# Kernel tuning notes

Hardware: AMD Instinct MI355X
Metric: run time of the kernel (lower is better)

## Reference

```python
import jax, jax.numpy as jnp
import numpy as np

D = 4096       # hidden_dim
L = 4          # num_iter
NEG = -1e9     # masked-softmax fill


def setup_inputs() -> dict:
    key = jax.random.key(0)
    ks = jax.random.split(key, 7)
    s_d = 1.0 / np.sqrt(D)
    s_2d = 1.0 / np.sqrt(2 * D)
    pi = np.float32(np.pi)
    concept_embed = jax.random.normal(ks[0], (54, D), jnp.float32)
    gat_W  = jax.random.normal(ks[1], (L, D, D), jnp.float32) * s_d     # HieGAT linear (no bias)
    att_if = jax.random.normal(ks[2], (L, 2 * D), jnp.float32) * s_2d   # Linear(2D,1) weight as vector
    att_fd = jax.random.normal(ks[3], (L, 2 * D), jnp.float32) * s_2d
    att_dr = jax.random.normal(ks[4], (L, 2 * D), jnp.float32) * s_2d
    meta_W = jax.random.normal(ks[5], (L, D, D), jnp.float32) * s_d     # MetapathAggr linear
    edge_embed = jax.random.uniform(ks[6], (3, D // 2), jnp.float32, minval=-pi, maxval=pi)
    # tree_structure[2] = [3,2,3,2,2] (facets per domain), tree_structure[3] = [3]*12 (ideos per facet)
    parent_of_facet = jnp.asarray(np.repeat(np.arange(5), [3, 2, 3, 2, 2]), jnp.int32)   # [12]
    parent_of_ideo = jnp.asarray(np.repeat(np.arange(12), 3), jnp.int32)                 # [36]
    return dict(concept_embed=concept_embed, gat_W=gat_W, att_if=att_if, att_fd=att_fd,
                att_dr=att_dr, meta_W=meta_W, edge_embed=edge_embed,
                parent_of_facet=parent_of_facet, parent_of_ideo=parent_of_ideo)


def _leaky(x):
    return jnp.where(x > 0, x, 0.01 * x)


def _attn_level(center, children, parent_idx, w):
    # center [P,D], children [C,D], parent_idx [C] -> aggregated centers [P,D]
    P = center.shape[0]
    s_self = _leaky(jnp.concatenate([center, center], axis=1) @ w)                 # [P]
    s_child = _leaky(jnp.concatenate([center[parent_idx], children], axis=1) @ w)  # [C]
    mask = parent_idx[None, :] == jnp.arange(P)[:, None]                           # [P,C]
    scores = jnp.concatenate([s_self[:, None], jnp.where(mask, s_child[None, :], NEG)], axis=1)
    a = jax.nn.softmax(scores, axis=1)                                             # [P,C+1]
    return a[:, :1] * center + a[:, 1:] @ children


def reference(concept_embed, gat_W, att_if, att_fd, att_dr, meta_W, edge_embed,
              parent_of_facet, parent_of_ideo):
    e_r, e_i = jnp.cos(edge_embed), jnp.sin(edge_embed)   # [3, D/2]
    pf = parent_of_facet
    pi_ = parent_of_ideo
    x = concept_embed
    for i in range(gat_W.shape[0]):
        # --- HieGAT layer: bottom-up attention aggregation ---
        h = x @ gat_W[i].T                                 # [54,D]
        root, dom, fac, ideo = h[0:1], h[1:6], h[6:18], h[18:54]
        fac_new = _attn_level(fac, ideo, pi_, att_if[i])
        dom_new = _attn_level(dom, fac_new, pf, att_fd[i])
        root_new = _attn_level(root, dom_new, jnp.zeros(5, jnp.int32), att_dr[i])
        x = jnp.concatenate([root_new, dom_new, fac_new, ideo], axis=0)
        # --- Metapath aggregation: top-down complex rotations ---
        h = x @ meta_W[i].T                                # [54,D]
        hr, hi = jnp.split(h, 2, axis=1)                   # each [54, D/2]
        rr, ri = hr[0:1], hi[0:1]
        dr = hr[1:6] + (rr * e_r[0] - ri * e_i[0])
        di = hi[1:6] + (rr * e_i[0] + ri * e_r[0])
        fr = hr[6:18] + (dr[pf] * e_r[1] - di[pf] * e_i[1])
        fi = hi[6:18] + (dr[pf] * e_i[1] + di[pf] * e_r[1])
        ir = hr[18:54] + (fr[pi_] * e_r[2] - fi[pi_] * e_i[2])
        ii = hi[18:54] + (fr[pi_] * e_i[2] + fi[pi_] * e_r[2])
        x = jnp.concatenate([
            h[0:1],
            jnp.concatenate([dr, di], axis=1) / 2,
            jnp.concatenate([fr, fi], axis=1) / 3,
            jnp.concatenate([ir, ii], axis=1) / 4,
        ], axis=0)
    return x
```

## Files before the change

### kernel.cpp

```cpp
#include <hip/hip_runtime.h>
#include <hip/hip_bf16.h>

#define DIM 4096
#define HROWS 54
#define HSZ (54 * 4096)
#define SPLITK 16
#define KSLICE 256

typedef __attribute__((ext_vector_type(4))) float  f32x4;
typedef __attribute__((ext_vector_type(8))) short  s16x8;
typedef __attribute__((ext_vector_type(4))) short  s16x4;

__device__ __forceinline__ short f2bf(float f) {
    union { __hip_bfloat16 h; short s; } u;
    u.h = __float2bfloat16(f);
    return u.s;
}
__device__ __forceinline__ float bf2f(short s) {
    union { __hip_bfloat16 h; short s; } u;
    u.s = s;
    return __bfloat162float(u.h);
}
__device__ __forceinline__ float leaky(float x) { return x > 0.f ? x : 0.01f * x; }

__device__ __forceinline__ void split8(const f32x4& c0, const f32x4& c1,
                                       s16x8& h, s16x8& l) {
#pragma unroll
    for (int j = 0; j < 4; ++j) {
        short h0 = f2bf(c0[j]); h[j]     = h0; l[j]     = f2bf(c0[j] - bf2f(h0));
        short h1 = f2bf(c1[j]); h[4 + j] = h1; l[4 + j] = f2bf(c1[j] - bf2f(h1));
    }
}

__global__ __launch_bounds__(256) void prep_g(const float* __restrict__ ce,
                                              const float* __restrict__ edge,
                                              short* __restrict__ xh, short* __restrict__ xl,
                                              short* __restrict__ hbh, short* __restrict__ hbl,
                                              float* __restrict__ er, float* __restrict__ ei)
{
    const int idx = blockIdx.x * 256 + threadIdx.x;
    const int row = idx >> 12;
    if (row < HROWS) {
        const float v = ce[idx];
        const short h = f2bf(v);
        xh[idx] = h; xl[idx] = f2bf(v - bf2f(h));
    } else {
        xh[idx] = 0; xl[idx] = 0; hbh[idx] = 0; hbl[idx] = 0;
    }
    if (idx < 3 * 2048) {
        const float e = edge[idx];
        er[idx] = cosf(e);
        ei[idx] = sinf(e);
    }
}

__global__ __launch_bounds__(256) void gemm_g(const short* __restrict__ Ah,
                                              const short* __restrict__ Al,
                                              const float* __restrict__ W,
                                              float* __restrict__ outp)
{
    __shared__ short lhi[64 * 256];
    __shared__ short llo[64 * 256];

    const int tid  = threadIdx.x;
    const int lane = tid & 63;
    const int wv   = tid >> 6;
    const int nb   = blockIdx.x & 31;
    const int ks   = blockIdx.x >> 5;
    const int l15  = lane & 15;
    const int lk8  = lane >> 4;
    const int koff = ks * KSLICE;

    for (int u = tid; u < 64 * 32; u += 256) {
        const int row  = u >> 5;
        const int c    = u & 31;
        const int slot = c ^ (row & 7);
        *(s16x8*)&lhi[row * 256 + slot * 8] =
            *(const s16x8*)(Ah + (size_t)row * DIM + koff + c * 8);
        *(s16x8*)&llo[row * 256 + slot * 8] =
            *(const s16x8*)(Al + (size_t)row * DIM + koff + c * 8);
    }
    __syncthreads();

    const int ncolA = nb * 128 + wv * 16 + l15;
    const int ncolB = ncolA + 64;
    const float* wpA = W + (size_t)ncolA * DIM + koff + lk8 * 8;
    const float* wpB = W + (size_t)ncolB * DIM + koff + lk8 * 8;

    f32x4 accA0 = {0.f,0.f,0.f,0.f}, accA1 = {0.f,0.f,0.f,0.f};
    f32x4 accA2 = {0.f,0.f,0.f,0.f}, accA3 = {0.f,0.f,0.f,0.f};
    f32x4 accB0 = {0.f,0.f,0.f,0.f}, accB1 = {0.f,0.f,0.f,0.f};
    f32x4 accB2 = {0.f,0.f,0.f,0.f}, accB3 = {0.f,0.f,0.f,0.f};

#define WLD(P, KB)                                                           \
    const f32x4 P##a0 = *(const f32x4*)(wpA + (KB)*64);                      \
    const f32x4 P##a1 = *(const f32x4*)(wpA + (KB)*64 + 4);                  \
    const f32x4 P##a2 = *(const f32x4*)(wpA + (KB)*64 + 32);                 \
    const f32x4 P##a3 = *(const f32x4*)(wpA + (KB)*64 + 36);                 \
    const f32x4 P##b0 = *(const f32x4*)(wpB + (KB)*64);                      \
    const f32x4 P##b1 = *(const f32x4*)(wpB + (KB)*64 + 4);                  \
    const f32x4 P##b2 = *(const f32x4*)(wpB + (KB)*64 + 32);                 \
    const f32x4 P##b3 = *(const f32x4*)(wpB + (KB)*64 + 36);

#define CKK(WA0, WA1, WB0, WB1, KB, KK)                                      \
    {   const int sl_ = (((KB)*8 + (KK)*4 + lk8) ^ (l15 & 7)) * 8;           \
        const s16x8 a0h = *(const s16x8*)&lhi[( 0 + l15)*256 + sl_];         \
        const s16x8 a1h = *(const s16x8*)&lhi[(16 + l15)*256 + sl_];         \
        const s16x8 a2h = *(const s16x8*)&lhi[(32 + l15)*256 + sl_];         \
        const s16x8 a3h = *(const s16x8*)&lhi[(48 + l15)*256 + sl_];         \
        const s16x8 a0l = *(const s16x8*)&llo[( 0 + l15)*256 + sl_];         \
        const s16x8 a1l = *(const s16x8*)&llo[(16 + l15)*256 + sl_];         \
        const s16x8 a2l = *(const s16x8*)&llo[(32 + l15)*256 + sl_];         \
        const s16x8 a3l = *(const s16x8*)&llo[(48 + l15)*256 + sl_];         \
        s16x8 bhA, blA, bhB, blB;                                            \
        split8(WA0, WA1, bhA, blA);                                          \
        split8(WB0, WB1, bhB, blB);                                          \
        accA0 = __builtin_amdgcn_mfma_f32_16x16x32_bf16(a0h, bhA, accA0, 0, 0, 0); \
        accA1 = __builtin_amdgcn_mfma_f32_16x16x32_bf16(a1h, bhA, accA1, 0, 0, 0); \
        accA2 = __builtin_amdgcn_mfma_f32_16x16x32_bf16(a2h, bhA, accA2, 0, 0, 0); \
        accA3 = __builtin_amdgcn_mfma_f32_16x16x32_bf16(a3h, bhA, accA3, 0, 0, 0); \
        accA0 = __builtin_amdgcn_mfma_f32_16x16x32_bf16(a0l, bhA, accA0, 0, 0, 0); \
        accA1 = __builtin_amdgcn_mfma_f32_16x16x32_bf16(a1l, bhA, accA1, 0, 0, 0); \
        accA2 = __builtin_amdgcn_mfma_f32_16x16x32_bf16(a2l, bhA, accA2, 0, 0, 0); \
        accA3 = __builtin_amdgcn_mfma_f32_16x16x32_bf16(a3l, bhA, accA3, 0, 0, 0); \
        accA0 = __builtin_amdgcn_mfma_f32_16x16x32_bf16(a0h, blA, accA0, 0, 0, 0); \
        accA1 = __builtin_amdgcn_mfma_f32_16x16x32_bf16(a1h, blA, accA1, 0, 0, 0); \
        accA2 = __builtin_amdgcn_mfma_f32_16x16x32_bf16(a2h, blA, accA2, 0, 0, 0); \
        accA3 = __builtin_amdgcn_mfma_f32_16x16x32_bf16(a3h, blA, accA3, 0, 0, 0); \
        accB0 = __builtin_amdgcn_mfma_f32_16x16x32_bf16(a0h, bhB, accB0, 0, 0, 0); \
        accB1 = __builtin_amdgcn_mfma_f32_16x16x32_bf16(a1h, bhB, accB1, 0, 0, 0); \
        accB2 = __builtin_amdgcn_mfma_f32_16x16x32_bf16(a2h, bhB, accB2, 0, 0, 0); \
        accB3 = __builtin_amdgcn_mfma_f32_16x16x32_bf16(a3h, bhB, accB3, 0, 0, 0); \
        accB0 = __builtin_amdgcn_mfma_f32_16x16x32_bf16(a0l, bhB, accB0, 0, 0, 0); \
        accB1 = __builtin_amdgcn_mfma_f32_16x16x32_bf16(a1l, bhB, accB1, 0, 0, 0); \
        accB2 = __builtin_amdgcn_mfma_f32_16x16x32_bf16(a2l, bhB, accB2, 0, 0, 0); \
        accB3 = __builtin_amdgcn_mfma_f32_16x16x32_bf16(a3l, bhB, accB3, 0, 0, 0); \
        accB0 = __builtin_amdgcn_mfma_f32_16x16x32_bf16(a0h, blB, accB0, 0, 0, 0); \
        accB1 = __builtin_amdgcn_mfma_f32_16x16x32_bf16(a1h, blB, accB1, 0, 0, 0); \
        accB2 = __builtin_amdgcn_mfma_f32_16x16x32_bf16(a2h, blB, accB2, 0, 0, 0); \
        accB3 = __builtin_amdgcn_mfma_f32_16x16x32_bf16(a3h, blB, accB3, 0, 0, 0); }

    WLD(w0_, 0) WLD(w1_, 1)
    CKK(w0_a0, w0_a1, w0_b0, w0_b1, 0, 0)
    CKK(w0_a2, w0_a3, w0_b2, w0_b3, 0, 1)
    WLD(w2_, 2)
    CKK(w1_a0, w1_a1, w1_b0, w1_b1, 1, 0)
    CKK(w1_a2, w1_a3, w1_b2, w1_b3, 1, 1)
    WLD(w3_, 3)
    CKK(w2_a0, w2_a1, w2_b0, w2_b1, 2, 0)
    CKK(w2_a2, w2_a3, w2_b2, w2_b3, 2, 1)
    CKK(w3_a0, w3_a1, w3_b0, w3_b1, 3, 0)
    CKK(w3_a2, w3_a3, w3_b2, w3_b3, 3, 1)

#undef WLD
#undef CKK

    float* op = outp + (size_t)ks * HSZ;
#pragma unroll
    for (int mt = 0; mt < 4; ++mt) {
        const f32x4 a = (mt == 0) ? accA0 : (mt == 1) ? accA1 : (mt == 2) ? accA2 : accA3;
        const f32x4 b = (mt == 0) ? accB0 : (mt == 1) ? accB1 : (mt == 2) ? accB2 : accB3;
#pragma unroll
        for (int r = 0; r < 4; ++r) {
            const int m = mt * 16 + lk8 * 4 + r;
            if (m < HROWS) {
                op[(size_t)m * DIM + ncolA] = a[r];
                op[(size_t)m * DIM + ncolB] = b[r];
            }
        }
    }
}

__global__ __launch_bounds__(256) void p2_g(const float* __restrict__ hpart,
                                            const float* __restrict__ wA,
                                            const float* __restrict__ wB,
                                            const float* __restrict__ wC,
                                            short* __restrict__ hbh, short* __restrict__ hbl,
                                            float* __restrict__ dotp)
{
    const int vb  = blockIdx.x;
    const int tid = threadIdx.x;
    const int i   = vb * 1024 + tid * 4;
    const int col = i & (DIM - 1);
    f32x4 s = {0.f,0.f,0.f,0.f};
#pragma unroll
    for (int sl = 0; sl < SPLITK; ++sl) s += *(const f32x4*)(hpart + (size_t)sl * HSZ + i);

    s16x4 vh, vl;
#pragma unroll
    for (int j = 0; j < 4; ++j) {
        const short h = f2bf(s[j]);
        vh[j] = h; vl[j] = f2bf(s[j] - bf2f(h));
    }
    *(s16x4*)(hbh + i) = vh;
    *(s16x4*)(hbl + i) = vl;

    float a0=0,a1=0,a2=0,a3=0,a4=0,a5=0;
#pragma unroll
    for (int j = 0; j < 4; ++j) {
        const float sv = s[j];
        const int c = col + j;
        a0 += sv * wA[c]; a1 += sv * wA[DIM + c];
        a2 += sv * wB[c]; a3 += sv * wB[DIM + c];
        a4 += sv * wC[c]; a5 += sv * wC[DIM + c];
    }
#pragma unroll
    for (int off = 32; off > 0; off >>= 1) {
        a0 += __shfl_down(a0, off); a1 += __shfl_down(a1, off);
        a2 += __shfl_down(a2, off); a3 += __shfl_down(a3, off);
        a4 += __shfl_down(a4, off); a5 += __shfl_down(a5, off);
    }
    if ((tid & 63) == 0) {
        float* d = dotp + ((size_t)vb * 4 + (tid >> 6)) * 6;
        d[0]=a0; d[1]=a1; d[2]=a2; d[3]=a3; d[4]=a4; d[5]=a5;
    }
}

__global__ __launch_bounds__(256) void p45_g(const float* __restrict__ hpart,
                                             const float* __restrict__ dotp,
                                             const float* __restrict__ er,
                                             const float* __restrict__ ei,
                                             short* __restrict__ xh, short* __restrict__ xl,
                                             float* __restrict__ xo, int last)
{
    const int b   = blockIdx.x;
    const int tid = threadIdx.x;
    __shared__ float gs[HROWS][16];
    __shared__ float ds[324];
    __shared__ float Ts[54][54];
    __shared__ float ad0[5], adc[12], ar[6], fdot3[12], fdot5[12], ddot5[5];

    for (int x = tid; x < HROWS * 16; x += 256) {
        const int row = x >> 4;
        const int c   = x & 15;
        const int gj  = (c < 8) ? (b * 8 + c) : (2048 + b * 8 + (c - 8));
        float s = 0.f;
#pragma unroll
        for (int sl = 0; sl < SPLITK; ++sl)
            s += hpart[(size_t)sl * HSZ + (size_t)row * DIM + gj];
        gs[row][c] = s;
    }

    for (int x = tid; x < 324; x += 256) {
        const int r_ = x / 6, v = x % 6;
        float s = 0.f;
#pragma unroll
        for (int u = 0; u < 16; ++u) s += dotp[(size_t)(r_ * 16 + u) * 6 + v];
        ds[x] = s;
    }
    for (int i = tid; i < 54 * 54; i += 256) ((float*)Ts)[i] = 0.f;
    __syncthreads();

    if (tid < 12) {
        const int p = tid;
        const float u = ds[(6+p)*6 + 0];
        const float ss = leaky(u + ds[(6+p)*6 + 1]);
        float sc[3], mx = ss;
#pragma unroll
        for (int j = 0; j < 3; ++j) { sc[j] = leaky(u + ds[(18+3*p+j)*6 + 1]); mx = fmaxf(mx, sc[j]); }
        float e0 = expf(ss - mx), s = e0, ec[3];
#pragma unroll
        for (int j = 0; j < 3; ++j) { ec[j] = expf(sc[j] - mx); s += ec[j]; }
        const float inv = 1.f / s;
        const float a0 = e0 * inv;
        float f3 = a0 * ds[(6+p)*6 + 3];
        float f5 = a0 * ds[(6+p)*6 + 5];
        Ts[6+p][6+p] = a0;
#pragma unroll
        for (int j = 0; j < 3; ++j) {
            const float a = ec[j] * inv;
            Ts[6+p][18+3*p+j] = a;
            f3 += a * ds[(18+3*p+j)*6 + 3];
            f5 += a * ds[(18+3*p+j)*6 + 5];
        }
        fdot3[p] = f3; fdot5[p] = f5;
    }
    __syncthreads();

    if (tid < 5) {
        const int p = tid;
        const int cstart[5] = {0,3,5,8,10};
        const int ccnt[5]   = {3,2,3,2,2};
        const float u = ds[(1+p)*6 + 2];
        const float ss = leaky(u + ds[(1+p)*6 + 3]);
        const int n = ccnt[p], c0 = cstart[p];
        float mx = ss, sc[3];
        for (int j = 0; j < n; ++j) { sc[j] = leaky(u + fdot3[c0+j]); mx = fmaxf(mx, sc[j]); }
        float e0 = expf(ss - mx), s = e0, ec[3];
        for (int j = 0; j < n; ++j) { ec[j] = expf(sc[j] - mx); s += ec[j]; }
        const float inv = 1.f / s;
        ad0[p] = e0 * inv;
        float d5 = ad0[p] * ds[(1+p)*6 + 5];
        for (int j = 0; j < n; ++j) {
            const float a = ec[j] * inv;
            adc[c0+j] = a;
            d5 += a * fdot5[c0+j];
        }
        ddot5[p] = d5;
    }
    __syncthreads();

    if (tid == 0) {
        const float u = ds[0*6 + 4];
        const float ss = leaky(u + ds[0*6 + 5]);
        float mx = ss, sc[5];
#pragma unroll
        for (int d = 0; d < 5; ++d) { sc[d] = leaky(u + ddot5[d]); mx = fmaxf(mx, sc[d]); }
        float e0 = expf(ss - mx), s = e0, ec[5];
#pragma unroll
        for (int d = 0; d < 5; ++d) { ec[d] = expf(sc[d] - mx); s += ec[d]; }
        const float inv = 1.f / s;
        ar[0] = e0 * inv;
#pragma unroll
        for (int d = 0; d < 5; ++d) ar[1+d] = ec[d] * inv;
    }
    for (int q = tid; q < 36; q += 256) Ts[18+q][18+q] = 1.f;
    __syncthreads();

    if (tid < 54) {
        const int j = tid;
        const int cstart[5] = {0,3,5,8,10};
        const int ccnt[5]   = {3,2,3,2,2};
        for (int p = 0; p < 5; ++p) {
            float t = ad0[p] * ((j == 1+p) ? 1.f : 0.f);
            for (int c = cstart[p]; c < cstart[p] + ccnt[p]; ++c) t += adc[c] * Ts[6+c][j];
            Ts[1+p][j] = t;
        }
    }
    __syncthreads();
    if (tid < 54) {
        float t = ar[0] * ((tid == 0) ? 1.f : 0.f);
        for (int d = 0; d < 5; ++d) t += ar[1+d] * Ts[1+d][tid];
        Ts[0][tid] = t;
    }
    __syncthreads();

    const int p  = tid & 7;
    const int rq = tid >> 3;
    const int j  = b * 8 + p;
    const int jj = j + 2048;
    constexpr int PF[12] = {0,0,0,1,1,2,2,2,3,3,4,4};

    const float er0 = er[j],        ei0 = ei[j];
    const float er1 = er[2048 + j], ei1 = ei[2048 + j];
    const float er2 = er[4096 + j], ei2 = ei[4096 + j];

    float a0r = 0.f, a0i = 0.f;
#pragma unroll 6
    for (int k = 0; k < HROWS; ++k) {
        const float t0 = Ts[0][k];
        a0r += t0 * gs[k][p];
        a0i += t0 * gs[k][p + 8];
    }
    const float rr = a0r, ri = a0i;

    for (int r = rq; r < HROWS; r += 32) {
        float vr, vi, scale;
        if (r == 0) {
            vr = rr; vi = ri; scale = 1.f;
        } else {
            int row1, row2 = 0;
            if (r < 6)       { row1 = r; }
            else if (r < 18) { const int c = r - 6;      row1 = 1 + PF[c]; row2 = r; }
            else             { const int c = (r - 18)/3; row1 = 1 + PF[c]; row2 = 6 + c; }

            float a1r = 0.f, a1i = 0.f;
#pragma unroll 6
            for (int k = 0; k < HROWS; ++k) {
                const float t1 = Ts[row1][k];
                a1r += t1 * gs[k][p];
                a1i += t1 * gs[k][p + 8];
            }
            const float dr = a1r + rr * er0 - ri * ei0;
            const float di = a1i + rr * ei0 + ri * er0;
            if (r < 6) {
                vr = dr; vi = di; scale = 0.5f;
            } else {
                float a2r = 0.f, a2i = 0.f;
#pragma unroll 6
                for (int k = 0; k < HROWS; ++k) {
                    const float t2 = Ts[row2][k];
                    a2r += t2 * gs[k][p];
                    a2i += t2 * gs[k][p + 8];
                }
                const float fr = a2r + dr * er1 - di * ei1;
                const float fi = a2i + dr * ei1 + di * er1;
                if (r < 18) {
                    vr = fr; vi = fi; scale = 1.f / 3.f;
                } else {
                    vr = gs[r][p]     + fr * er2 - fi * ei2;
                    vi = gs[r][p + 8] + fr * ei2 + fi * er2;
                    scale = 0.25f;
                }
            }
        }
        vr *= scale; vi *= scale;
        if (last) {
            xo[(size_t)r * DIM + j]  = vr;
            xo[(size_t)r * DIM + jj] = vi;
        } else {
            const short h0 = f2bf(vr);
            xh[(size_t)r * DIM + j] = h0;
            xl[(size_t)r * DIM + j] = f2bf(vr - bf2f(h0));
            const short h1 = f2bf(vi);
            xh[(size_t)r * DIM + jj] = h1;
            xl[(size_t)r * DIM + jj] = f2bf(vi - bf2f(h1));
        }
    }
}

extern "C" void kernel_launch(void* const* d_in, const int* in_sizes, int n_in,
                              void* d_out, int out_size, void* d_ws, size_t ws_size,
                              hipStream_t stream)
{
    const float* ce    = (const float*)d_in[0];
    const float* gatW  = (const float*)d_in[1];
    const float* attif = (const float*)d_in[2];
    const float* attfd = (const float*)d_in[3];
    const float* attdr = (const float*)d_in[4];
    const float* metaW = (const float*)d_in[5];
    const float* edge  = (const float*)d_in[6];
    float* out = (float*)d_out;

    char* w = (char*)d_ws;
    float* hpart = (float*)w;   w += (size_t)SPLITK * HSZ * 4;
    float* dotp  = (float*)w;   w += 6144 * 4;
    float* er    = (float*)w;   w += 3 * 2048 * 4;
    float* ei    = (float*)w;   w += 3 * 2048 * 4;
    short* xbfh  = (short*)w;   w += (size_t)64 * DIM * 2;
    short* xbfl  = (short*)w;   w += (size_t)64 * DIM * 2;
    short* hbfh  = (short*)w;   w += (size_t)64 * DIM * 2;
    short* hbfl  = (short*)w;   w += (size_t)64 * DIM * 2;

    hipLaunchKernelGGL(prep_g, dim3(1024), dim3(256), 0, stream,
                       ce, edge, xbfh, xbfl, hbfh, hbfl, er, ei);

    for (int i = 0; i < 4; ++i) {
        hipLaunchKernelGGL(gemm_g, dim3(512), dim3(256), 0, stream,
                           xbfh, xbfl, gatW + (size_t)i * DIM * DIM, hpart);
        hipLaunchKernelGGL(p2_g, dim3(216), dim3(256), 0, stream,
                           hpart, attif + (size_t)i * 2 * DIM, attfd + (size_t)i * 2 * DIM,
                           attdr + (size_t)i * 2 * DIM, hbfh, hbfl, dotp);
        hipLaunchKernelGGL(gemm_g, dim3(512), dim3(256), 0, stream,
                           hbfh, hbfl, metaW + (size_t)i * DIM * DIM, hpart);
        hipLaunchKernelGGL(p45_g, dim3(256), dim3(256), 0, stream,
                           hpart, dotp, er, ei, xbfh, xbfl, out, (i == 3) ? 1 : 0);
    }
}
```

Measured before the change: 259.0 us.

## Fuse activation bf16 split into GEMM staging, halve split-K, drop prep kernel

The GEMM now reads fp32 activations directly and does the hi/lo bf16 split while staging into shared memory. The prep kernel and the separate bf16 activation buffers are removed, and cos/sin of the edge embeddings are computed inside p45. Split-K drops from 16 to 8 and each block covers 64 columns over a 512-wide K slice in two staged halves, which halves the partial-sum traffic reduced in p2/p45. The cost is redundant split work across the 64 column blocks, fp32 activation reads that are twice as wide, extra syncs, and fewer accumulators per wave.

```diff
diff --git a/kernel.cpp b/kernel.cpp
--- a/kernel.cpp
+++ b/kernel.cpp
@@ -4,12 +4,11 @@
 #define DIM 4096
 #define HROWS 54
 #define HSZ (54 * 4096)
-#define SPLITK 16
-#define KSLICE 256
+#define SPLITK 8
+#define KSLICE 512
 
 typedef __attribute__((ext_vector_type(4))) float  f32x4;
 typedef __attribute__((ext_vector_type(8))) short  s16x8;
-typedef __attribute__((ext_vector_type(4))) short  s16x4;
 
 __device__ __forceinline__ short f2bf(float f) {
     union { __hip_bfloat16 h; short s; } u;
@@ -32,30 +31,7 @@
     }
 }
 
-__global__ __launch_bounds__(256) void prep_g(const float* __restrict__ ce,
-                                              const float* __restrict__ edge,
-                                              short* __restrict__ xh, short* __restrict__ xl,
-                                              short* __restrict__ hbh, short* __restrict__ hbl,
-                                              float* __restrict__ er, float* __restrict__ ei)
-{
-    const int idx = blockIdx.x * 256 + threadIdx.x;
-    const int row = idx >> 12;
-    if (row < HROWS) {
-        const float v = ce[idx];
-        const short h = f2bf(v);
-        xh[idx] = h; xl[idx] = f2bf(v - bf2f(h));
-    } else {
-        xh[idx] = 0; xl[idx] = 0; hbh[idx] = 0; hbl[idx] = 0;
-    }
-    if (idx < 3 * 2048) {
-        const float e = edge[idx];
-        er[idx] = cosf(e);
-        ei[idx] = sinf(e);
-    }
-}
-
-__global__ __launch_bounds__(256) void gemm_g(const short* __restrict__ Ah,
-                                              const short* __restrict__ Al,
+__global__ __launch_bounds__(256) void gemm_g(const float* __restrict__ Asrc,
                                               const float* __restrict__ W,
                                               float* __restrict__ outp)
 {
@@ -65,108 +41,94 @@
     const int tid  = threadIdx.x;
     const int lane = tid & 63;
     const int wv   = tid >> 6;
-    const int nb   = blockIdx.x & 31;
-    const int ks   = blockIdx.x >> 5;
+    const int nb   = blockIdx.x & 63;
+    const int ks   = blockIdx.x >> 6;
     const int l15  = lane & 15;
     const int lk8  = lane >> 4;
     const int koff = ks * KSLICE;
 
-    for (int u = tid; u < 64 * 32; u += 256) {
-        const int row  = u >> 5;
-        const int c    = u & 31;
-        const int slot = c ^ (row & 7);
-        *(s16x8*)&lhi[row * 256 + slot * 8] =
-            *(const s16x8*)(Ah + (size_t)row * DIM + koff + c * 8);
-        *(s16x8*)&llo[row * 256 + slot * 8] =
-            *(const s16x8*)(Al + (size_t)row * DIM + koff + c * 8);
-    }
-    __syncthreads();
-
-    const int ncolA = nb * 128 + wv * 16 + l15;
-    const int ncolB = ncolA + 64;
-    const float* wpA = W + (size_t)ncolA * DIM + koff + lk8 * 8;
-    const float* wpB = W + (size_t)ncolB * DIM + koff + lk8 * 8;
-
-    f32x4 accA0 = {0.f,0.f,0.f,0.f}, accA1 = {0.f,0.f,0.f,0.f};
-    f32x4 accA2 = {0.f,0.f,0.f,0.f}, accA3 = {0.f,0.f,0.f,0.f};
-    f32x4 accB0 = {0.f,0.f,0.f,0.f}, accB1 = {0.f,0.f,0.f,0.f};
-    f32x4 accB2 = {0.f,0.f,0.f,0.f}, accB3 = {0.f,0.f,0.f,0.f};
-
-#define WLD(P, KB)                                                           \
-    const f32x4 P##a0 = *(const f32x4*)(wpA + (KB)*64);                      \
-    const f32x4 P##a1 = *(const f32x4*)(wpA + (KB)*64 + 4);                  \
-    const f32x4 P##a2 = *(const f32x4*)(wpA + (KB)*64 + 32);                 \
-    const f32x4 P##a3 = *(const f32x4*)(wpA + (KB)*64 + 36);                 \
-    const f32x4 P##b0 = *(const f32x4*)(wpB + (KB)*64);                      \
-    const f32x4 P##b1 = *(const f32x4*)(wpB + (KB)*64 + 4);                  \
-    const f32x4 P##b2 = *(const f32x4*)(wpB + (KB)*64 + 32);                 \
-    const f32x4 P##b3 = *(const f32x4*)(wpB + (KB)*64 + 36);
-
-#define CKK(WA0, WA1, WB0, WB1, KB, KK)                                      \
-    {   const int sl_ = (((KB)*8 + (KK)*4 + lk8) ^ (l15 & 7)) * 8;           \
-        const s16x8 a0h = *(const s16x8*)&lhi[( 0 + l15)*256 + sl_];         \
-        const s16x8 a1h = *(const s16x8*)&lhi[(16 + l15)*256 + sl_];         \
-        const s16x8 a2h = *(const s16x8*)&lhi[(32 + l15)*256 + sl_];         \
-        const s16x8 a3h = *(const s16x8*)&lhi[(48 + l15)*256 + sl_];         \
-        const s16x8 a0l = *(const s16x8*)&llo[( 0 + l15)*256 + sl_];         \
-        const s16x8 a1l = *(const s16x8*)&llo[(16 + l15)*256 + sl_];         \
-        const s16x8 a2l = *(const s16x8*)&llo[(32 + l15)*256 + sl_];         \
-        const s16x8 a3l = *(const s16x8*)&llo[(48 + l15)*256 + sl_];         \
-        s16x8 bhA, blA, bhB, blB;                                            \
-        split8(WA0, WA1, bhA, blA);                                          \
-        split8(WB0, WB1, bhB, blB);                                          \
-        accA0 = __builtin_amdgcn_mfma_f32_16x16x32_bf16(a0h, bhA, accA0, 0, 0, 0); \
-        accA1 = __builtin_amdgcn_mfma_f32_16x16x32_bf16(a1h, bhA, accA1, 0, 0, 0); \
-        accA2 = __builtin_amdgcn_mfma_f32_16x16x32_bf16(a2h, bhA, accA2, 0, 0, 0); \
-        accA3 = __builtin_amdgcn_mfma_f32_16x16x32_bf16(a3h, bhA, accA3, 0, 0, 0); \
-        accA0 = __builtin_amdgcn_mfma_f32_16x16x32_bf16(a0l, bhA, accA0, 0, 0, 0); \
-        accA1 = __builtin_amdgcn_mfma_f32_16x16x32_bf16(a1l, bhA, accA1, 0, 0, 0); \
-        accA2 = __builtin_amdgcn_mfma_f32_16x16x32_bf16(a2l, bhA, accA2, 0, 0, 0); \
-        accA3 = __builtin_amdgcn_mfma_f32_16x16x32_bf16(a3l, bhA, accA3, 0, 0, 0); \
-        accA0 = __builtin_amdgcn_mfma_f32_16x16x32_bf16(a0h, blA, accA0, 0, 0, 0); \
-        accA1 = __builtin_amdgcn_mfma_f32_16x16x32_bf16(a1h, blA, accA1, 0, 0, 0); \
-        accA2 = __builtin_amdgcn_mfma_f32_16x16x32_bf16(a2h, blA, accA2, 0, 0, 0); \
-        accA3 = __builtin_amdgcn_mfma_f32_16x16x32_bf16(a3h, blA, accA3, 0, 0, 0); \
-        accB0 = __builtin_amdgcn_mfma_f32_16x16x32_bf16(a0h, bhB, accB0, 0, 0, 0); \
-        accB1 = __builtin_amdgcn_mfma_f32_16x16x32_bf16(a1h, bhB, accB1, 0, 0, 0); \
-        accB2 = __builtin_amdgcn_mfma_f32_16x16x32_bf16(a2h, bhB, accB2, 0, 0, 0); \
-        accB3 = __builtin_amdgcn_mfma_f32_16x16x32_bf16(a3h, bhB, accB3, 0, 0, 0); \
-        accB0 = __builtin_amdgcn_mfma_f32_16x16x32_bf16(a0l, bhB, accB0, 0, 0, 0); \
-        accB1 = __builtin_amdgcn_mfma_f32_16x16x32_bf16(a1l, bhB, accB1, 0, 0, 0); \
-        accB2 = __builtin_amdgcn_mfma_f32_16x16x32_bf16(a2l, bhB, accB2, 0, 0, 0); \
-        accB3 = __builtin_amdgcn_mfma_f32_16x16x32_bf16(a3l, bhB, accB3, 0, 0, 0); \
-        accB0 = __builtin_amdgcn_mfma_f32_16x16x32_bf16(a0h, blB, accB0, 0, 0, 0); \
-        accB1 = __builtin_amdgcn_mfma_f32_16x16x32_bf16(a1h, blB, accB1, 0, 0, 0); \
-        accB2 = __builtin_amdgcn_mfma_f32_16x16x32_bf16(a2h, blB, accB2, 0, 0, 0); \
-        accB3 = __builtin_amdgcn_mfma_f32_16x16x32_bf16(a3h, blB, accB3, 0, 0, 0); }
-
-    WLD(w0_, 0) WLD(w1_, 1)
-    CKK(w0_a0, w0_a1, w0_b0, w0_b1, 0, 0)
-    CKK(w0_a2, w0_a3, w0_b2, w0_b3, 0, 1)
-    WLD(w2_, 2)
-    CKK(w1_a0, w1_a1, w1_b0, w1_b1, 1, 0)
-    CKK(w1_a2, w1_a3, w1_b2, w1_b3, 1, 1)
+    const int ncol = nb * 64 + wv * 16 + l15;
+    const float* wp = W + (size_t)ncol * DIM + koff + lk8 * 8;
+
+    f32x4 acc0 = {0.f,0.f,0.f,0.f}, acc1 = {0.f,0.f,0.f,0.f};
+    f32x4 acc2 = {0.f,0.f,0.f,0.f}, acc3 = {0.f,0.f,0.f,0.f};
+
+#define STAGEA(HALF)                                                          \
+    for (int u = tid; u < 64 * 32; u += 256) {                                \
+        const int row  = u >> 5;                                              \
+        const int c    = u & 31;                                              \
+        const int slot = c ^ (row & 7);                                       \
+        f32x4 a0 = {0.f,0.f,0.f,0.f}, a1 = {0.f,0.f,0.f,0.f};                 \
+        if (row < HROWS) {                                                    \
+            const float* g = Asrc + (size_t)row * DIM + koff + (HALF)*256 + c*8; \
+            a0 = *(const f32x4*)g;  a1 = *(const f32x4*)(g + 4);              \
+        }                                                                     \
+        s16x8 vh, vl; split8(a0, a1, vh, vl);                                 \
+        *(s16x8*)&lhi[row * 256 + slot * 8] = vh;                             \
+        *(s16x8*)&llo[row * 256 + slot * 8] = vl;                             \
+    }
+
+#define WLD(P, KB)                                                            \
+    const f32x4 P##0 = *(const f32x4*)(wp + (KB)*64);                         \
+    const f32x4 P##1 = *(const f32x4*)(wp + (KB)*64 + 4);                     \
+    const f32x4 P##2 = *(const f32x4*)(wp + (KB)*64 + 32);                    \
+    const f32x4 P##3 = *(const f32x4*)(wp + (KB)*64 + 36);
+
+#define CKK(W0, W1, KBL, KK)                                                  \
+    {   const int sl_ = (((KBL)*8 + (KK)*4 + lk8) ^ (l15 & 7)) * 8;           \
+        const s16x8 a0h = *(const s16x8*)&lhi[( 0 + l15)*256 + sl_];          \
+        const s16x8 a1h = *(const s16x8*)&lhi[(16 + l15)*256 + sl_];          \
+        const s16x8 a2h = *(const s16x8*)&lhi[(32 + l15)*256 + sl_];          \
+        const s16x8 a3h = *(const s16x8*)&lhi[(48 + l15)*256 + sl_];          \
+        const s16x8 a0l = *(const s16x8*)&llo[( 0 + l15)*256 + sl_];          \
+        const s16x8 a1l = *(const s16x8*)&llo[(16 + l15)*256 + sl_];          \
+        const s16x8 a2l = *(const s16x8*)&llo[(32 + l15)*256 + sl_];          \
+        const s16x8 a3l = *(const s16x8*)&llo[(48 + l15)*256 + sl_];          \
+        s16x8 bh, bl; split8(W0, W1, bh, bl);                                 \
+        acc0 = __builtin_amdgcn_mfma_f32_16x16x32_bf16(a0h, bh, acc0, 0, 0, 0); \
+        acc1 = __builtin_amdgcn_mfma_f32_16x16x32_bf16(a1h, bh, acc1, 0, 0, 0); \
+        acc2 = __builtin_amdgcn_mfma_f32_16x16x32_bf16(a2h, bh, acc2, 0, 0, 0); \
+        acc3 = __builtin_amdgcn_mfma_f32_16x16x32_bf16(a3h, bh, acc3, 0, 0, 0); \
+        acc0 = __builtin_amdgcn_mfma_f32_16x16x32_bf16(a0l, bh, acc0, 0, 0, 0); \
+        acc1 = __builtin_amdgcn_mfma_f32_16x16x32_bf16(a1l, bh, acc1, 0, 0, 0); \
+        acc2 = __builtin_amdgcn_mfma_f32_16x16x32_bf16(a2l, bh, acc2, 0, 0, 0); \
+        acc3 = __builtin_amdgcn_mfma_f32_16x16x32_bf16(a3l, bh, acc3, 0, 0, 0); \
+        acc0 = __builtin_amdgcn_mfma_f32_16x16x32_bf16(a0h, bl, acc0, 0, 0, 0); \
+        acc1 = __builtin_amdgcn_mfma_f32_16x16x32_bf16(a1h, bl, acc1, 0, 0, 0); \
+        acc2 = __builtin_amdgcn_mfma_f32_16x16x32_bf16(a2h, bl, acc2, 0, 0, 0); \
+        acc3 = __builtin_amdgcn_mfma_f32_16x16x32_bf16(a3h, bl, acc3, 0, 0, 0); }
+
+    STAGEA(0)
+    __syncthreads();
+    WLD(w0_, 0) WLD(w1_, 1) WLD(w2_, 2)
+    CKK(w0_0, w0_1, 0, 0) CKK(w0_2, w0_3, 0, 1)
     WLD(w3_, 3)
-    CKK(w2_a0, w2_a1, w2_b0, w2_b1, 2, 0)
-    CKK(w2_a2, w2_a3, w2_b2, w2_b3, 2, 1)
-    CKK(w3_a0, w3_a1, w3_b0, w3_b1, 3, 0)
-    CKK(w3_a2, w3_a3, w3_b2, w3_b3, 3, 1)
-
+    CKK(w1_0, w1_1, 1, 0) CKK(w1_2, w1_3, 1, 1)
+    CKK(w2_0, w2_1, 2, 0) CKK(w2_2, w2_3, 2, 1)
+    CKK(w3_0, w3_1, 3, 0) CKK(w3_2, w3_3, 3, 1)
+    __syncthreads();
+    WLD(w4_, 4) WLD(w5_, 5)
+    STAGEA(1)
+    __syncthreads();
+    WLD(w6_, 6)
+    CKK(w4_0, w4_1, 0, 0) CKK(w4_2, w4_3, 0, 1)
+    WLD(w7_, 7)
+    CKK(w5_0, w5_1, 1, 0) CKK(w5_2, w5_3, 1, 1)
+    CKK(w6_0, w6_1, 2, 0) CKK(w6_2, w6_3, 2, 1)
+    CKK(w7_0, w7_1, 3, 0) CKK(w7_2, w7_3, 3, 1)
+
+#undef STAGEA
 #undef WLD
 #undef CKK
 
     float* op = outp + (size_t)ks * HSZ;
 #pragma unroll
     for (int mt = 0; mt < 4; ++mt) {
-        const f32x4 a = (mt == 0) ? accA0 : (mt == 1) ? accA1 : (mt == 2) ? accA2 : accA3;
-        const f32x4 b = (mt == 0) ? accB0 : (mt == 1) ? accB1 : (mt == 2) ? accB2 : accB3;
+        const f32x4 a = (mt == 0) ? acc0 : (mt == 1) ? acc1 : (mt == 2) ? acc2 : acc3;
 #pragma unroll
         for (int r = 0; r < 4; ++r) {
             const int m = mt * 16 + lk8 * 4 + r;
-            if (m < HROWS) {
-                op[(size_t)m * DIM + ncolA] = a[r];
-                op[(size_t)m * DIM + ncolB] = b[r];
-            }
+            if (m < HROWS) op[(size_t)m * DIM + ncol] = a[r];
         }
     }
 }
@@ -175,7 +137,7 @@
                                             const float* __restrict__ wA,
                                             const float* __restrict__ wB,
                                             const float* __restrict__ wC,
-                                            short* __restrict__ hbh, short* __restrict__ hbl,
+                                            float* __restrict__ hout,
                                             float* __restrict__ dotp)
 {
     const int vb  = blockIdx.x;
@@ -186,14 +148,7 @@
 #pragma unroll
     for (int sl = 0; sl < SPLITK; ++sl) s += *(const f32x4*)(hpart + (size_t)sl * HSZ + i);
 
-    s16x4 vh, vl;
-#pragma unroll
-    for (int j = 0; j < 4; ++j) {
-        const short h = f2bf(s[j]);
-        vh[j] = h; vl[j] = f2bf(s[j] - bf2f(h));
-    }
-    *(s16x4*)(hbh + i) = vh;
-    *(s16x4*)(hbl + i) = vl;
+    *(f32x4*)(hout + i) = s;
 
     float a0=0,a1=0,a2=0,a3=0,a4=0,a5=0;
 #pragma unroll
@@ -218,9 +173,8 @@
 
 __global__ __launch_bounds__(256) void p45_g(const float* __restrict__ hpart,
                                              const float* __restrict__ dotp,
-                                             const float* __restrict__ er,
-                                             const float* __restrict__ ei,
-                                             short* __restrict__ xh, short* __restrict__ xl,
+                                             const float* __restrict__ edge,
+                                             float* __restrict__ xf,
                                              float* __restrict__ xo, int last)
 {
     const int b   = blockIdx.x;
@@ -341,9 +295,10 @@
     const int jj = j + 2048;
     constexpr int PF[12] = {0,0,0,1,1,2,2,2,3,3,4,4};
 
-    const float er0 = er[j],        ei0 = ei[j];
-    const float er1 = er[2048 + j], ei1 = ei[2048 + j];
-    const float er2 = er[4096 + j], ei2 = ei[4096 + j];
+    const float e0 = edge[j], e1 = edge[2048 + j], e2 = edge[4096 + j];
+    const float er0 = cosf(e0), ei0 = sinf(e0);
+    const float er1 = cosf(e1), ei1 = sinf(e1);
+    const float er2 = cosf(e2), ei2 = sinf(e2);
 
     float a0r = 0.f, a0i = 0.f;
 #pragma unroll 6
@@ -395,17 +350,9 @@
             }
         }
         vr *= scale; vi *= scale;
-        if (last) {
-            xo[(size_t)r * DIM + j]  = vr;
-            xo[(size_t)r * DIM + jj] = vi;
-        } else {
-            const short h0 = f2bf(vr);
-            xh[(size_t)r * DIM + j] = h0;
-            xl[(size_t)r * DIM + j] = f2bf(vr - bf2f(h0));
-            const short h1 = f2bf(vi);
-            xh[(size_t)r * DIM + jj] = h1;
-            xl[(size_t)r * DIM + jj] = f2bf(vi - bf2f(h1));
-        }
+        float* dst = last ? xo : xf;
+        dst[(size_t)r * DIM + j]  = vr;
+        dst[(size_t)r * DIM + jj] = vi;
     }
 }
 
@@ -424,26 +371,19 @@
 
     char* w = (char*)d_ws;
     float* hpart = (float*)w;   w += (size_t)SPLITK * HSZ * 4;
+    float* hf    = (float*)w;   w += (size_t)HSZ * 4;
+    float* xf    = (float*)w;   w += (size_t)HSZ * 4;
     float* dotp  = (float*)w;   w += 6144 * 4;
-    float* er    = (float*)w;   w += 3 * 2048 * 4;
-    float* ei    = (float*)w;   w += 3 * 2048 * 4;
-    short* xbfh  = (short*)w;   w += (size_t)64 * DIM * 2;
-    short* xbfl  = (short*)w;   w += (size_t)64 * DIM * 2;
-    short* hbfh  = (short*)w;   w += (size_t)64 * DIM * 2;
-    short* hbfl  = (short*)w;   w += (size_t)64 * DIM * 2;
-
-    hipLaunchKernelGGL(prep_g, dim3(1024), dim3(256), 0, stream,
-                       ce, edge, xbfh, xbfl, hbfh, hbfl, er, ei);
 
     for (int i = 0; i < 4; ++i) {
         hipLaunchKernelGGL(gemm_g, dim3(512), dim3(256), 0, stream,
-                           xbfh, xbfl, gatW + (size_t)i * DIM * DIM, hpart);
+                           (i == 0) ? ce : xf, gatW + (size_t)i * DIM * DIM, hpart);
         hipLaunchKernelGGL(p2_g, dim3(216), dim3(256), 0, stream,
                            hpart, attif + (size_t)i * 2 * DIM, attfd + (size_t)i * 2 * DIM,
-                           attdr + (size_t)i * 2 * DIM, hbfh, hbfl, dotp);
+                           attdr + (size_t)i * 2 * DIM, hf, dotp);
         hipLaunchKernelGGL(gemm_g, dim3(512), dim3(256), 0, stream,
-                           hbfh, hbfl, metaW + (size_t)i * DIM * DIM, hpart);
+                           hf, metaW + (size_t)i * DIM * DIM, hpart);
         hipLaunchKernelGGL(p45_g, dim3(256), dim3(256), 0, stream,
-                           hpart, dotp, er, ei, xbfh, xbfl, out, (i == 3) ? 1 : 0);
-    }
-}
+                           hpart, dotp, edge, xf, out, (i == 3) ? 1 : 0);
+    }
+}
```

Result: slower. 329.5 us (+27.2%).

## Drop prep kernel, fuse input split into first GEMM, swizzle GEMM blocks

Applied to the files above, without the earlier changes.

Removes the separate prep launch. The first GAT GEMM now reads the fp32 concept embeddings directly and splits them into bf16 hi/lo inside its shared-memory staging. cos/sin of the edge embeddings are recomputed per thread in p45 instead of being read from a precomputed buffer. The GEMM block index is also swizzled to change the order in which blocks read W tiles, and the split-K partial reduction in p45 is vectorized to f32x4 loads. The zero-fill of the bf16 padding rows (54–63) is no longer done; this relies on those rows only feeding output rows that are never stored.

```diff
diff --git a/kernel.cpp b/kernel.cpp
--- a/kernel.cpp
+++ b/kernel.cpp
@@ -32,55 +32,16 @@
     }
 }
 
-__global__ __launch_bounds__(256) void prep_g(const float* __restrict__ ce,
-                                              const float* __restrict__ edge,
-                                              short* __restrict__ xh, short* __restrict__ xl,
-                                              short* __restrict__ hbh, short* __restrict__ hbl,
-                                              float* __restrict__ er, float* __restrict__ ei)
-{
-    const int idx = blockIdx.x * 256 + threadIdx.x;
-    const int row = idx >> 12;
-    if (row < HROWS) {
-        const float v = ce[idx];
-        const short h = f2bf(v);
-        xh[idx] = h; xl[idx] = f2bf(v - bf2f(h));
-    } else {
-        xh[idx] = 0; xl[idx] = 0; hbh[idx] = 0; hbl[idx] = 0;
-    }
-    if (idx < 3 * 2048) {
-        const float e = edge[idx];
-        er[idx] = cosf(e);
-        ei[idx] = sinf(e);
-    }
-}
-
-__global__ __launch_bounds__(256) void gemm_g(const short* __restrict__ Ah,
-                                              const short* __restrict__ Al,
-                                              const float* __restrict__ W,
-                                              float* __restrict__ outp)
-{
-    __shared__ short lhi[64 * 256];
-    __shared__ short llo[64 * 256];
-
-    const int tid  = threadIdx.x;
+__device__ __forceinline__ void gemm_core(const short* lhi, const short* llo,
+                                          const float* __restrict__ W,
+                                          float* __restrict__ outp,
+                                          int tid, int nb, int ks)
+{
     const int lane = tid & 63;
     const int wv   = tid >> 6;
-    const int nb   = blockIdx.x & 31;
-    const int ks   = blockIdx.x >> 5;
     const int l15  = lane & 15;
     const int lk8  = lane >> 4;
     const int koff = ks * KSLICE;
-
-    for (int u = tid; u < 64 * 32; u += 256) {
-        const int row  = u >> 5;
-        const int c    = u & 31;
-        const int slot = c ^ (row & 7);
-        *(s16x8*)&lhi[row * 256 + slot * 8] =
-            *(const s16x8*)(Ah + (size_t)row * DIM + koff + c * 8);
-        *(s16x8*)&llo[row * 256 + slot * 8] =
-            *(const s16x8*)(Al + (size_t)row * DIM + koff + c * 8);
-    }
-    __syncthreads();
 
     const int ncolA = nb * 128 + wv * 16 + l15;
     const int ncolB = ncolA + 64;
@@ -171,6 +132,66 @@
     }
 }
 
+__global__ __launch_bounds__(256) void gemm_bf_g(const short* __restrict__ Ah,
+                                                 const short* __restrict__ Al,
+                                                 const float* __restrict__ W,
+                                                 float* __restrict__ outp)
+{
+    __shared__ short lhi[64 * 256];
+    __shared__ short llo[64 * 256];
+
+    const int tid = threadIdx.x;
+    const int bid = blockIdx.x;
+    const int swz = (bid & 7) * 64 + (bid >> 3);
+    const int nb  = swz & 31;
+    const int ks  = swz >> 5;
+    const int koff = ks * KSLICE;
+
+    for (int u = tid; u < 64 * 32; u += 256) {
+        const int row  = u >> 5;
+        const int c    = u & 31;
+        const int slot = c ^ (row & 7);
+        *(s16x8*)&lhi[row * 256 + slot * 8] =
+            *(const s16x8*)(Ah + (size_t)row * DIM + koff + c * 8);
+        *(s16x8*)&llo[row * 256 + slot * 8] =
+            *(const s16x8*)(Al + (size_t)row * DIM + koff + c * 8);
+    }
+    __syncthreads();
+    gemm_core(lhi, llo, W, outp, tid, nb, ks);
+}
+
+__global__ __launch_bounds__(256) void gemm_f32_g(const float* __restrict__ Asrc,
+                                                  const float* __restrict__ W,
+                                                  float* __restrict__ outp)
+{
+    __shared__ short lhi[64 * 256];
+    __shared__ short llo[64 * 256];
+
+    const int tid = threadIdx.x;
+    const int bid = blockIdx.x;
+    const int swz = (bid & 7) * 64 + (bid >> 3);
+    const int nb  = swz & 31;
+    const int ks  = swz >> 5;
+    const int koff = ks * KSLICE;
+
+    for (int u = tid; u < 64 * 32; u += 256) {
+        const int row  = u >> 5;
+        const int c    = u & 31;
+        const int slot = c ^ (row & 7);
+        f32x4 a0 = {0.f,0.f,0.f,0.f}, a1 = {0.f,0.f,0.f,0.f};
+        if (row < HROWS) {
+            const float* g = Asrc + (size_t)row * DIM + koff + c * 8;
+            a0 = *(const f32x4*)g;
+            a1 = *(const f32x4*)(g + 4);
+        }
+        s16x8 vh, vl; split8(a0, a1, vh, vl);
+        *(s16x8*)&lhi[row * 256 + slot * 8] = vh;
+        *(s16x8*)&llo[row * 256 + slot * 8] = vl;
+    }
+    __syncthreads();
+    gemm_core(lhi, llo, W, outp, tid, nb, ks);
+}
+
 __global__ __launch_bounds__(256) void p2_g(const float* __restrict__ hpart,
                                             const float* __restrict__ wA,
                                             const float* __restrict__ wB,
@@ -218,8 +239,7 @@
 
 __global__ __launch_bounds__(256) void p45_g(const float* __restrict__ hpart,
                                              const float* __restrict__ dotp,
-                                             const float* __restrict__ er,
-                                             const float* __restrict__ ei,
+                                             const float* __restrict__ edge,
                                              short* __restrict__ xh, short* __restrict__ xl,
                                              float* __restrict__ xo, int last)
 {
@@ -230,15 +250,15 @@
     __shared__ float Ts[54][54];
     __shared__ float ad0[5], adc[12], ar[6], fdot3[12], fdot5[12], ddot5[5];
 
-    for (int x = tid; x < HROWS * 16; x += 256) {
-        const int row = x >> 4;
-        const int c   = x & 15;
-        const int gj  = (c < 8) ? (b * 8 + c) : (2048 + b * 8 + (c - 8));
-        float s = 0.f;
+    if (tid < 216) {
+        const int row = tid >> 2;
+        const int ch  = tid & 3;
+        const int gj  = (ch < 2) ? (b * 8 + ch * 4) : (2048 + b * 8 + (ch - 2) * 4);
+        f32x4 s = {0.f,0.f,0.f,0.f};
 #pragma unroll
         for (int sl = 0; sl < SPLITK; ++sl)
-            s += hpart[(size_t)sl * HSZ + (size_t)row * DIM + gj];
-        gs[row][c] = s;
+            s += *(const f32x4*)(hpart + (size_t)sl * HSZ + (size_t)row * DIM + gj);
+        *(f32x4*)&gs[row][(ch & 1) * 4 + (ch >> 1) * 8] = s;
     }
 
     for (int x = tid; x < 324; x += 256) {
@@ -341,9 +361,10 @@
     const int jj = j + 2048;
     constexpr int PF[12] = {0,0,0,1,1,2,2,2,3,3,4,4};
 
-    const float er0 = er[j],        ei0 = ei[j];
-    const float er1 = er[2048 + j], ei1 = ei[2048 + j];
-    const float er2 = er[4096 + j], ei2 = ei[4096 + j];
+    const float e0v = edge[j], e1v = edge[2048 + j], e2v = edge[4096 + j];
+    const float er0 = cosf(e0v), ei0 = sinf(e0v);
+    const float er1 = cosf(e1v), ei1 = sinf(e1v);
+    const float er2 = cosf(e2v), ei2 = sinf(e2v);
 
     float a0r = 0.f, a0i = 0.f;
 #pragma unroll 6
@@ -425,25 +446,24 @@
     char* w = (char*)d_ws;
     float* hpart = (float*)w;   w += (size_t)SPLITK * HSZ * 4;
     float* dotp  = (float*)w;   w += 6144 * 4;
-    float* er    = (float*)w;   w += 3 * 2048 * 4;
-    float* ei    = (float*)w;   w += 3 * 2048 * 4;
     short* xbfh  = (short*)w;   w += (size_t)64 * DIM * 2;
     short* xbfl  = (short*)w;   w += (size_t)64 * DIM * 2;
     short* hbfh  = (short*)w;   w += (size_t)64 * DIM * 2;
     short* hbfl  = (short*)w;   w += (size_t)64 * DIM * 2;
 
-    hipLaunchKernelGGL(prep_g, dim3(1024), dim3(256), 0, stream,
-                       ce, edge, xbfh, xbfl, hbfh, hbfl, er, ei);
-
     for (int i = 0; i < 4; ++i) {
-        hipLaunchKernelGGL(gemm_g, dim3(512), dim3(256), 0, stream,
-                           xbfh, xbfl, gatW + (size_t)i * DIM * DIM, hpart);
+        if (i == 0)
+            hipLaunchKernelGGL(gemm_f32_g, dim3(512), dim3(256), 0, stream,
+                               ce, gatW, hpart);
+        else
+            hipLaunchKernelGGL(gemm_bf_g, dim3(512), dim3(256), 0, stream,
+                               xbfh, xbfl, gatW + (size_t)i * DIM * DIM, hpart);
         hipLaunchKernelGGL(p2_g, dim3(216), dim3(256), 0, stream,
                            hpart, attif + (size_t)i * 2 * DIM, attfd + (size_t)i * 2 * DIM,
                            attdr + (size_t)i * 2 * DIM, hbfh, hbfl, dotp);
-        hipLaunchKernelGGL(gemm_g, dim3(512), dim3(256), 0, stream,
+        hipLaunchKernelGGL(gemm_bf_g, dim3(512), dim3(256), 0, stream,
                            hbfh, hbfl, metaW + (size_t)i * DIM * DIM, hpart);
         hipLaunchKernelGGL(p45_g, dim3(256), dim3(256), 0, stream,
-                           hpart, dotp, er, ei, xbfh, xbfl, out, (i == 3) ? 1 : 0);
-    }
-}
+                           hpart, dotp, edge, xbfh, xbfl, out, (i == 3) ? 1 : 0);
+    }
+}
```

Measured after the change: 260.8 us. About the same (+0.7%).
